# Optimization experiments

Hardware: AMD Instinct MI355X
Metric: run time of the kernel (lower is better)

The kernel has to match this reference:

```python
import jax, jax.numpy as jnp
import numpy as np

EOS_IDX = 2
B, S, T = 512, 64, 32
V, E, H, DENC, L = 128, 256, 512, 1024, 2


def setup_inputs() -> dict:
    key = jax.random.key(0)
    ks = jax.random.split(key, 24)
    s = 0.02
    inp = {
        "encoder_out": jax.random.normal(ks[0], (B, S, DENC), jnp.float32),
        "h0": jax.random.normal(ks[1], (L, B, H), jnp.float32),
        "c0": jax.random.normal(ks[2], (L, B, H), jnp.float32),
        "targets": jax.random.randint(ks[3], (B, T), 0, V),
        "mask": jax.random.randint(ks[4], (B, S), 0, 2).astype(jnp.int32),
        # parameters
        "emb": jax.random.normal(ks[5], (V, E), jnp.float32) * s,
        "W_enc": jax.random.normal(ks[6], (H, DENC), jnp.float32) * s,
        "W_dec": jax.random.normal(ks[7], (H, H), jnp.float32) * s,
        "v": jax.random.normal(ks[8], (H,), jnp.float32) * s,
        "W_ih0": jax.random.normal(ks[9], (4 * H, E + DENC), jnp.float32) * s,
        "W_hh0": jax.random.normal(ks[10], (4 * H, H), jnp.float32) * s,
        "b_ih0": jax.random.normal(ks[11], (4 * H,), jnp.float32) * s,
        "b_hh0": jax.random.normal(ks[12], (4 * H,), jnp.float32) * s,
        "W_ih1": jax.random.normal(ks[13], (4 * H, H), jnp.float32) * s,
        "W_hh1": jax.random.normal(ks[14], (4 * H, H), jnp.float32) * s,
        "b_ih1": jax.random.normal(ks[15], (4 * H,), jnp.float32) * s,
        "b_hh1": jax.random.normal(ks[16], (4 * H,), jnp.float32) * s,
        "W_out": jax.random.normal(ks[17], (V, H + DENC + E), jnp.float32) * s,
        "b_out": jax.random.normal(ks[18], (V,), jnp.float32) * s,
    }
    # guarantee at least one valid source position per row
    inp["mask"] = inp["mask"].at[:, 0].set(1)
    return inp


def _lstm_cell(x, h, c, W_ih, W_hh, b_ih, b_hh):
    gates = x @ W_ih.T + b_ih + h @ W_hh.T + b_hh  # (B, 4H)
    i, f, g, o = jnp.split(gates, 4, axis=-1)      # torch gate order i,f,g,o
    c_new = jax.nn.sigmoid(f) * c + jax.nn.sigmoid(i) * jnp.tanh(g)
    h_new = jax.nn.sigmoid(o) * jnp.tanh(c_new)
    return h_new, c_new


def reference(encoder_out, h0, c0, targets, mask,
              emb, W_enc, W_dec, v,
              W_ih0, W_hh0, b_ih0, b_hh0,
              W_ih1, W_hh1, b_ih1, b_hh1,
              W_out, b_out):
    # teacher_forcing_ratio = 1.0: input tokens are [EOS, targets[:, :-1]]
    tokens = jnp.concatenate(
        [jnp.full((targets.shape[0], 1), EOS_IDX, dtype=targets.dtype),
         targets[:, :-1]], axis=1)                       # (B, T)
    embedded = emb[tokens]                               # (B, T, E)
    enc_proj = jnp.einsum('bsd,hd->bsh', encoder_out, W_enc)  # precompute W_enc(encoder_out)
    mask_b = mask > 0                                    # (B, S)

    def step(carry, x_emb):                              # x_emb: (B, E)
        h, c = carry                                     # each (L, B, H)
        h_top = h[-1]                                    # (B, H)
        dec_proj = h_top @ W_dec.T                       # (B, H)
        energy = jnp.tanh(dec_proj[:, None, :] + enc_proj)   # (B, S, H)
        score = jnp.einsum('bsh,h->bs', energy, v)       # (B, S)
        score = jnp.where(mask_b, score, -jnp.inf)
        weights = jax.nn.softmax(score, axis=-1)         # (B, S)
        context = jnp.einsum('bs,bsd->bd', weights, encoder_out)  # (B, DENC)
        x = jnp.concatenate([x_emb, context], axis=-1)   # (B, E+DENC)
        h0n, c0n = _lstm_cell(x, h[0], c[0], W_ih0, W_hh0, b_ih0, b_hh0)
        h1n, c1n = _lstm_cell(h0n, h[1], c[1], W_ih1, W_hh1, b_ih1, b_hh1)
        pred = jnp.concatenate([h1n, context, x_emb], axis=-1) @ W_out.T + b_out  # (B, V)
        return (jnp.stack([h0n, h1n]), jnp.stack([c0n, c1n])), pred

    (_, _), preds = jax.lax.scan(step, (h0, c0), jnp.swapaxes(embedded, 0, 1))
    return jnp.swapaxes(preds, 0, 1)                     # (B, T, V)
```

## Files before the change

### kernel.cpp

```cpp
#include <hip/hip_runtime.h>
#include <math.h>

#define BB 512
#define SS 64
#define TT 32
#define VV 128
#define EE 256
#define HH 512
#define DENC 1024
#define BH (BB*HH)
#define XW0 1792
#define XW1 1024
#define PW  1792
#define G4H 2048

typedef __attribute__((ext_vector_type(8))) short bf16x8;
typedef __attribute__((ext_vector_type(4))) short bf16x4;
typedef __attribute__((ext_vector_type(4))) float f32x4;

__device__ __forceinline__ float sigf(float x){ return 1.f/(1.f+expf(-x)); }
__device__ __forceinline__ float bf2f(short s){
  return __uint_as_float(((unsigned)(unsigned short)s) << 16);
}
__device__ __forceinline__ short f2bf(float f){
  unsigned u = __float_as_uint(f);
  return (short)((u + 0x7FFF + ((u>>16)&1)) >> 16);
}
__device__ __forceinline__ float tanh_fast(float x){
  x = fminf(fmaxf(x, -15.f), 15.f);
  float e = __expf(2.f*x);
  return (e - 1.f) / (e + 1.f);
}

template<int BM, int BN>
struct GemmPipe {
  static constexpr int LA = 72;
  static __device__ __forceinline__ void run(short* Asb, short* Bsb,
      const short* __restrict__ A, const short* __restrict__ Bt, int K,
      int rowBase, int colBase, int tid, f32x4 acc[BM/32][BN/32])
  {
    constexpr int FI = BM/32, FJ = BN/32, ACH = BM/32, BCH = BN/32;
    const int lane = tid & 63, wave = tid >> 6;
    const int ml = lane & 15, kq = lane >> 4;
    const int wm = (wave >> 1)*(BM/2), wn = (wave & 1)*(BN/2);
    const int arow = (tid*ACH) >> 3, acol = ((tid*ACH) & 7)*8;
    const int brow = (tid*BCH) >> 3, bcol = ((tid*BCH) & 7)*8;
    const short* Ap = A + (size_t)(rowBase+arow)*K + acol;
    const short* Bp = Bt + (size_t)(colBase+brow)*K + bcol;
    bf16x8 ar[ACH], br[BCH];
    #pragma unroll
    for (int c = 0; c < ACH; ++c) ar[c] = *(const bf16x8*)(Ap + c*8);
    #pragma unroll
    for (int c = 0; c < BCH; ++c) br[c] = *(const bf16x8*)(Bp + c*8);
    const int nIter = K >> 6;
    for (int i = 0; i < nIter; ++i) {
      short* Ab = Asb + (i&1)*(BM*LA);
      short* Bb = Bsb + (i&1)*(BN*LA);
      #pragma unroll
      for (int c = 0; c < ACH; ++c) *(bf16x8*)&Ab[arow*LA + acol + c*8] = ar[c];
      #pragma unroll
      for (int c = 0; c < BCH; ++c) *(bf16x8*)&Bb[brow*LA + bcol + c*8] = br[c];
      __syncthreads();
      if (i+1 < nIter) {
        const short* An = Ap + (size_t)(i+1)*64;
        const short* Bn = Bp + (size_t)(i+1)*64;
        #pragma unroll
        for (int c = 0; c < ACH; ++c) ar[c] = *(const bf16x8*)(An + c*8);
        #pragma unroll
        for (int c = 0; c < BCH; ++c) br[c] = *(const bf16x8*)(Bn + c*8);
      }
      #pragma unroll
      for (int kh = 0; kh < 2; ++kh) {
        bf16x8 af[FI], bfv[FJ];
        #pragma unroll
        for (int ii = 0; ii < FI; ++ii)
          af[ii] = *(const bf16x8*)&Ab[(wm + ii*16 + ml)*LA + kh*32 + kq*8];
        #pragma unroll
        for (int jj = 0; jj < FJ; ++jj)
          bfv[jj] = *(const bf16x8*)&Bb[(wn + jj*16 + ml)*LA + kh*32 + kq*8];
        #pragma unroll
        for (int ii = 0; ii < FI; ++ii)
          #pragma unroll
          for (int jj = 0; jj < FJ; ++jj)
            acc[ii][jj] = __builtin_amdgcn_mfma_f32_16x16x32_bf16(af[ii], bfv[jj], acc[ii][jj], 0,0,0);
      }
    }
    __syncthreads();
  }
};

__global__ __launch_bounds__(256)
void gates_fused(const short* __restrict__ A, const short* __restrict__ W,
                 const float* __restrict__ bias, float* __restrict__ cb,
                 short* __restrict__ d1, short* __restrict__ d2, short* __restrict__ d3,
                 int K, int layer)
{
  __shared__ __align__(16) char smem[36864];
  short* As = (short*)smem;
  short* Bs = (short*)(smem + 18432);
  const int tid = threadIdx.x;
  const int rowBase = blockIdx.y*64, colBase = blockIdx.x*64;
  f32x4 acc[2][2];
  #pragma unroll
  for (int i = 0; i < 2; ++i)
    #pragma unroll
    for (int j = 0; j < 2; ++j) acc[i][j] = {0.f,0.f,0.f,0.f};
  GemmPipe<64,64>::run(As, Bs, A, W, K, rowBase, colBase, tid, acc);
  const int lane = tid & 63, wave = tid >> 6, ml = lane & 15, kq = lane >> 4;
  const int wm = (wave >> 1)*32, wn = (wave & 1)*32;
  float* Ct = (float*)smem;
  float bj0 = bias[colBase + wn + ml];
  float bj1 = bias[colBase + wn + 16 + ml];
  #pragma unroll
  for (int ii = 0; ii < 2; ++ii)
    #pragma unroll
    for (int jj = 0; jj < 2; ++jj)
      #pragma unroll
      for (int r2 = 0; r2 < 4; ++r2)
        Ct[(wm + ii*16 + kq*4 + r2)*68 + wn + jj*16 + ml] = acc[ii][jj][r2] + (jj ? bj1 : bj0);
  __syncthreads();
  #pragma unroll
  for (int kk = 0; kk < 4; ++kk) {
    int cidx = tid + kk*256;
    int m = cidx >> 4, hl = cidx & 15;
    float4 gv = *(float4*)&Ct[m*68 + hl*4];
    int b_ = rowBase + m, h_ = (colBase >> 2) + hl;
    float cp = cb[b_*HH + h_];
    float cn = sigf(gv.y)*cp + sigf(gv.x)*tanhf(gv.z);
    float hn = sigf(gv.w)*tanhf(cn);
    cb[b_*HH + h_] = cn;
    short hb16 = f2bf(hn);
    if (layer == 0) {
      d1[(size_t)b_*XW1 + h_] = hb16;
      d2[(size_t)b_*XW0 + h_] = hb16;
    } else {
      d1[(size_t)b_*XW1 + h_] = hb16;
      d2[(size_t)b_*PW  + h_] = hb16;
      d3[(size_t)b_*HH  + h_] = hb16;
    }
  }
}

__global__ __launch_bounds__(256)
void attn_out(const short* __restrict__ enc_proj, const short* __restrict__ enc_out,
              const float* __restrict__ vvec, const int* __restrict__ mask,
              const int* __restrict__ targets, const short* __restrict__ embb,
              const short* __restrict__ hb, const short* __restrict__ wdecT,
              short* __restrict__ xcat0, short* __restrict__ predcat,
              const short* __restrict__ predprev, const short* __restrict__ wout,
              const float* __restrict__ b_out, float* __restrict__ out, int t)
{
  __shared__ __align__(16) char smem[36864];
  const int tid = threadIdx.x;
  if (blockIdx.x >= 256) {
    if (t == 0) return;
    short* As = (short*)smem;
    short* Bs = (short*)(smem + 18432);
    int idx = blockIdx.x - 256;
    int rowBase = (idx >> 1)*64, colBase = (idx & 1)*64;
    f32x4 acc[2][2];
    #pragma unroll
    for (int i = 0; i < 2; ++i)
      #pragma unroll
      for (int j = 0; j < 2; ++j) acc[i][j] = {0.f,0.f,0.f,0.f};
    GemmPipe<64,64>::run(As, Bs, predprev, wout, PW, rowBase, colBase, tid, acc);
    const int lane = tid & 63, wave = tid >> 6, ml = lane & 15, kq = lane >> 4;
    const int wm = (wave >> 1)*32, wn = (wave & 1)*32;
    #pragma unroll
    for (int ii = 0; ii < 2; ++ii)
      #pragma unroll
      for (int jj = 0; jj < 2; ++jj) {
        int n = colBase + wn + jj*16 + ml;
        float bv = b_out[n];
        #pragma unroll
        for (int r2 = 0; r2 < 4; ++r2) {
          int m = rowBase + wm + ii*16 + kq*4 + r2;
          out[(size_t)m*(TT*VV) + (size_t)(t-1)*VV + n] = acc[ii][jj][r2] + bv;
        }
      }
    return;
  }
  if (t >= TT) return;
  const int b0 = blockIdx.x*2;
  float* hbf = (float*)smem;
  float* dps = (float*)(smem + 4096);
  float* vvf = (float*)(smem + 12288);
  float* sc  = (float*)(smem + 14336);
  float* wt  = (float*)(smem + 14848);
  {
    bf16x4 h4 = *(const bf16x4*)&hb[(size_t)b0*HH + tid*4];
    #pragma unroll
    for (int j = 0; j < 4; ++j) hbf[tid*4 + j] = bf2f(h4[j]);
    vvf[tid] = vvec[tid];
    vvf[256 + tid] = vvec[256 + tid];
  }
  __syncthreads();
  {
    int unit = tid & 127, ksel = tid >> 7;
    int bb = unit >> 6, h8 = unit & 63;
    const short* wp = wdecT + (size_t)(ksel*256)*HH + h8*8;
    const float* hrow = hbf + bb*HH + ksel*256;
    float a[8] = {0.f,0.f,0.f,0.f,0.f,0.f,0.f,0.f};
    for (int k = 0; k < 256; ++k) {
      bf16x8 w8 = *(const bf16x8*)(wp + (size_t)k*HH);
      float x = hrow[k];
      #pragma unroll
      for (int j = 0; j < 8; ++j) a[j] += x * bf2f(w8[j]);
    }
    float* d = dps + (ksel*2 + bb)*HH + h8*8;
    #pragma unroll
    for (int j = 0; j < 8; ++j) d[j] = a[j];
  }
  __syncthreads();
  {
    int bb = tid >> 7, h0 = (tid & 127)*4;
    f32x4 s0 = *(f32x4*)&dps[bb*HH + h0];
    f32x4 s1 = *(f32x4*)&dps[(2 + bb)*HH + h0];
    *(f32x4*)&dps[bb*HH + h0] = s0 + s1;
  }
  __syncthreads();
  {
    int u = tid >> 1, khalf = tid & 1;
    int bb = u >> 6, s = u & 63;
    const short* ep = enc_proj + ((size_t)(b0+bb)*SS + s)*HH + khalf*256;
    const float* dpp = dps + bb*HH + khalf*256;
    const float* vp  = vvf + khalf*256;
    float accv = 0.f;
    for (int hc = 0; hc < 32; ++hc) {
      bf16x8 e8 = *(const bf16x8*)(ep + hc*8);
      f32x4 d0 = *(const f32x4*)(dpp + hc*8);
      f32x4 d1 = *(const f32x4*)(dpp + hc*8 + 4);
      f32x4 v0 = *(const f32x4*)(vp + hc*8);
      f32x4 v1 = *(const f32x4*)(vp + hc*8 + 4);
      #pragma unroll
      for (int j = 0; j < 4; ++j) accv += v0[j]*tanh_fast(d0[j] + bf2f(e8[j]));
      #pragma unroll
      for (int j = 0; j < 4; ++j) accv += v1[j]*tanh_fast(d1[j] + bf2f(e8[4+j]));
    }
    accv += __shfl_xor(accv, 1, 64);
    if (khalf == 0) sc[bb*64 + s] = accv;
  }
  __syncthreads();
  if (tid < 128) {
    int bb = tid >> 6, s = tid & 63;
    int valid = mask[(b0+bb)*SS + s];
    float x = valid ? sc[bb*64 + s] : -INFINITY;
    float mx = x;
    #pragma unroll
    for (int off = 32; off; off >>= 1) mx = fmaxf(mx, __shfl_xor(mx, off, 64));
    float e = valid ? __expf(x - mx) : 0.f;
    float sum = e;
    #pragma unroll
    for (int off = 32; off; off >>= 1) sum += __shfl_xor(sum, off, 64);
    wt[bb*64 + s] = e / sum;
  }
  __syncthreads();
  {
    int bb = tid >> 7, d0 = (tid & 127)*8;
    const short* eob = enc_out + (size_t)(b0+bb)*SS*DENC + d0;
    float ca[8] = {0.f,0.f,0.f,0.f,0.f,0.f,0.f,0.f};
    for (int s = 0; s < SS; ++s) {
      float w = wt[bb*64 + s];
      bf16x8 e8 = *(const bf16x8*)(eob + (size_t)s*DENC);
      #pragma unroll
      for (int j = 0; j < 8; ++j) ca[j] += w * bf2f(e8[j]);
    }
    bf16x8 cb8;
    #pragma unroll
    for (int j = 0; j < 8; ++j) cb8[j] = f2bf(ca[j]);
    int b_ = b0 + bb;
    *(bf16x8*)&xcat0[(size_t)b_*XW0 + EE + d0] = cb8;
    *(bf16x8*)&predcat[(size_t)b_*PW + HH + d0] = cb8;
  }
  #pragma unroll
  for (int bb = 0; bb < 2; ++bb) {
    int b_ = b0 + bb;
    int tok = (t == 0) ? 2 : targets[b_*TT + t - 1];
    short ev = embb[tok*EE + tid];
    xcat0[(size_t)b_*XW0 + tid] = ev;
    predcat[(size_t)b_*PW + HH + DENC + tid] = ev;
  }
}

__global__ __launch_bounds__(256)
void enc_gemm(short* __restrict__ C, const short* __restrict__ A, const short* __restrict__ Bt,
              int K, int ldc)
{
  __shared__ __align__(16) char smem[55296];
  short* As = (short*)smem;
  short* Bs = (short*)(smem + 18432);
  const int tid = threadIdx.x;
  const int rowBase = blockIdx.y*64, colBase = blockIdx.x*128;
  f32x4 acc[2][4];
  #pragma unroll
  for (int i = 0; i < 2; ++i)
    #pragma unroll
    for (int j = 0; j < 4; ++j) acc[i][j] = {0.f,0.f,0.f,0.f};
  GemmPipe<64,128>::run(As, Bs, A, Bt, K, rowBase, colBase, tid, acc);
  const int lane = tid & 63, wave = tid >> 6, ml = lane & 15, kq = lane >> 4;
  const int wm = (wave >> 1)*32, wn = (wave & 1)*64;
  #pragma unroll
  for (int ii = 0; ii < 2; ++ii)
    #pragma unroll
    for (int jj = 0; jj < 4; ++jj) {
      int n = colBase + wn + jj*16 + ml;
      #pragma unroll
      for (int r2 = 0; r2 < 4; ++r2) {
        int m = rowBase + wm + ii*16 + kq*4 + r2;
        C[(size_t)m*ldc + n] = f2bf(acc[ii][jj][r2]);
      }
    }
}

__global__ __launch_bounds__(256)
void build_wcat_bf(short* __restrict__ wcat0, short* __restrict__ wcat1,
                   const float* __restrict__ wih0, const float* __restrict__ whh0,
                   const float* __restrict__ wih1, const float* __restrict__ whh1)
{
  int idx = blockIdx.x*256 + threadIdx.x;
  const int N0 = G4H*XW0;
  if (idx < N0) {
    int n = idx / XW0, k = idx % XW0;
    int row = (n & 3)*HH + (n >> 2);
    float v = (k < EE+DENC) ? wih0[(size_t)row*(EE+DENC) + k] : whh0[(size_t)row*HH + (k - (EE+DENC))];
    wcat0[idx] = f2bf(v);
  } else {
    int j = idx - N0;
    int n = j / XW1, k = j % XW1;
    int row = (n & 3)*HH + (n >> 2);
    float v = (k < HH) ? wih1[(size_t)row*HH + k] : whh1[(size_t)row*HH + (k - HH)];
    wcat1[j] = f2bf(v);
  }
}

__global__ __launch_bounds__(256)
void cvt_encout(short* __restrict__ dst, const float* __restrict__ src)
{
  size_t i8 = ((size_t)blockIdx.x*256 + threadIdx.x)*8;
  float4 a = *(const float4*)&src[i8];
  float4 b = *(const float4*)&src[i8+4];
  bf16x8 o;
  o[0]=f2bf(a.x); o[1]=f2bf(a.y); o[2]=f2bf(a.z); o[3]=f2bf(a.w);
  o[4]=f2bf(b.x); o[5]=f2bf(b.y); o[6]=f2bf(b.z); o[7]=f2bf(b.w);
  *(bf16x8*)&dst[i8] = o;
}

__global__ __launch_bounds__(256)
void prep_misc(float* __restrict__ cbuf, short* __restrict__ xcat0a, short* __restrict__ xcat1a,
               short* __restrict__ hb, short* __restrict__ wdecT, short* __restrict__ wenc,
               short* __restrict__ wout, short* __restrict__ embb,
               float* __restrict__ bias0i, float* __restrict__ bias1i,
               const float* __restrict__ c0, const float* __restrict__ h0,
               const float* __restrict__ W_dec, const float* __restrict__ W_enc,
               const float* __restrict__ W_out, const float* __restrict__ emb,
               const float* __restrict__ b_ih0, const float* __restrict__ b_hh0,
               const float* __restrict__ b_ih1, const float* __restrict__ b_hh1)
{
  int idx = blockIdx.x*256 + threadIdx.x;
  if (idx < 524288) { cbuf[idx] = c0[idx]; return; }
  idx -= 524288;
  if (idx < 262144) {
    int b = idx >> 9, h = idx & 511;
    xcat0a[(size_t)b*XW0 + EE + DENC + h] = f2bf(h0[idx]);
    return;
  }
  idx -= 262144;
  if (idx < 262144) {
    int b = idx >> 9, h = idx & 511;
    short v = f2bf(h0[BH + idx]);
    xcat1a[(size_t)b*XW1 + HH + h] = v;
    hb[idx] = v;
    return;
  }
  idx -= 262144;
  if (idx < 262144) {
    int k = idx >> 9, n = idx & 511;
    wdecT[idx] = f2bf(W_dec[(size_t)n*HH + k]);
    return;
  }
  idx -= 262144;
  if (idx < 524288) { wenc[idx] = f2bf(W_enc[idx]); return; }
  idx -= 524288;
  if (idx < 229376) { wout[idx] = f2bf(W_out[idx]); return; }
  idx -= 229376;
  if (idx < 32768)  { embb[idx] = f2bf(emb[idx]); return; }
  idx -= 32768;
  if (idx < 2048) {
    int row = (idx & 3)*HH + (idx >> 2);
    bias0i[idx] = b_ih0[row] + b_hh0[row];
    return;
  }
  idx -= 2048;
  {
    int row = (idx & 3)*HH + (idx >> 2);
    bias1i[idx] = b_ih1[row] + b_hh1[row];
  }
}

extern "C" void kernel_launch(void* const* d_in, const int* in_sizes, int n_in,
                              void* d_out, int out_size, void* d_ws, size_t ws_size,
                              hipStream_t stream) {
  const float* enc_out = (const float*)d_in[0];
  const float* h0      = (const float*)d_in[1];
  const float* c0      = (const float*)d_in[2];
  const int*   targets = (const int*)d_in[3];
  const int*   mask    = (const int*)d_in[4];
  const float* emb     = (const float*)d_in[5];
  const float* W_enc   = (const float*)d_in[6];
  const float* W_dec   = (const float*)d_in[7];
  const float* v       = (const float*)d_in[8];
  const float* b_ih0   = (const float*)d_in[11];
  const float* b_hh0   = (const float*)d_in[12];
  const float* b_ih1   = (const float*)d_in[15];
  const float* b_hh1   = (const float*)d_in[16];
  const float* b_out   = (const float*)d_in[18];
  float* out = (float*)d_out;

  char* ws = (char*)d_ws;
  size_t o = 0;
  short* enc_out_bf = (short*)(ws + o); o += (size_t)BB*SS*DENC*2;
  short* enc_proj_bf= (short*)(ws + o); o += (size_t)BB*SS*HH*2;
  short* wcat0i     = (short*)(ws + o); o += (size_t)G4H*XW0*2;
  short* wcat1i     = (short*)(ws + o); o += (size_t)G4H*XW1*2;
  short* wdecT      = (short*)(ws + o); o += (size_t)HH*HH*2;
  short* wenc_bf    = (short*)(ws + o); o += (size_t)HH*DENC*2;
  short* wout_bf    = (short*)(ws + o); o += (size_t)VV*PW*2;
  short* emb_bf     = (short*)(ws + o); o += (size_t)VV*EE*2;
  short* xcat0a     = (short*)(ws + o); o += (size_t)BB*XW0*2;
  short* xcat0b     = (short*)(ws + o); o += (size_t)BB*XW0*2;
  short* xcat1a     = (short*)(ws + o); o += (size_t)BB*XW1*2;
  short* xcat1b     = (short*)(ws + o); o += (size_t)BB*XW1*2;
  short* predcata   = (short*)(ws + o); o += (size_t)BB*PW*2;
  short* predcatb   = (short*)(ws + o); o += (size_t)BB*PW*2;
  short* hb         = (short*)(ws + o); o += (size_t)BH*2;
  float* cbuf       = (float*)(ws + o); o += (size_t)2*BH*4;
  float* bias0i     = (float*)(ws + o); o += (size_t)G4H*4;
  float* bias1i     = (float*)(ws + o); o += (size_t)G4H*4;
  (void)ws_size; (void)in_sizes; (void)n_in; (void)out_size;

  cvt_encout<<<16384, 256, 0, stream>>>(enc_out_bf, enc_out);
  build_wcat_bf<<<22528, 256, 0, stream>>>(wcat0i, wcat1i,
      (const float*)d_in[9], (const float*)d_in[10], (const float*)d_in[13], (const float*)d_in[14]);
  prep_misc<<<8208, 256, 0, stream>>>(cbuf, xcat0a, xcat1a, hb, wdecT, wenc_bf, wout_bf, emb_bf,
      bias0i, bias1i, c0, h0, W_dec, W_enc, (const float*)d_in[17], emb,
      b_ih0, b_hh0, b_ih1, b_hh1);
  enc_gemm<<<dim3(HH/128, (BB*SS)/64), 256, 0, stream>>>(
      enc_proj_bf, enc_out_bf, wenc_bf, DENC, HH);

  short* xc0[2] = {xcat0a, xcat0b};
  short* xc1[2] = {xcat1a, xcat1b};
  short* pc[2]  = {predcata, predcatb};
  for (int t = 0; t < TT; ++t) {
    attn_out<<<272, 256, 0, stream>>>(enc_proj_bf, enc_out_bf, v, mask, targets, emb_bf,
        hb, wdecT, xc0[t&1], pc[t&1], pc[(t+1)&1], wout_bf, b_out, out, t);
    gates_fused<<<dim3(G4H/64, BB/64), 256, 0, stream>>>(
        xc0[t&1], wcat0i, bias0i, cbuf, xc1[t&1], xc0[(t+1)&1] + EE + DENC, (short*)nullptr, XW0, 0);
    gates_fused<<<dim3(G4H/64, BB/64), 256, 0, stream>>>(
        xc1[t&1], wcat1i, bias1i, cbuf + BH, xc1[(t+1)&1] + HH, pc[t&1], hb, XW1, 1);
  }
  attn_out<<<272, 256, 0, stream>>>(enc_proj_bf, enc_out_bf, v, mask, targets, emb_bf,
      hb, wdecT, xc0[0], pc[0], pc[1], wout_bf, b_out, out, TT);
}
```

Baseline: 2.868 ms.

## Fuse decoder time loop into one persistent kernel with grid barriers

Replaces the 97 per-step kernel launches with a single persistent kernel of 256 blocks that runs all 32 timesteps. Phases are separated by an atomic-counter grid barrier. The output projection is reworked into a split-K MFMA over 16x16 tiles so it maps onto the same 256 blocks. The aim is to remove launch overhead and inter-kernel gaps on this latency-bound recurrence. In exchange it relies on all 256 blocks being co-resident and adds barrier spin cost at each phase.

```diff
diff --git a/kernel.cpp b/kernel.cpp
--- a/kernel.cpp
+++ b/kernel.cpp
@@ -30,6 +30,23 @@
   x = fminf(fmaxf(x, -15.f), 15.f);
   float e = __expf(2.f*x);
   return (e - 1.f) / (e + 1.f);
+}
+
+__device__ __forceinline__ void gridbar(unsigned* cnt, unsigned* gen)
+{
+  __syncthreads();
+  if (threadIdx.x == 0) {
+    unsigned g = __hip_atomic_load(gen, __ATOMIC_RELAXED, __HIP_MEMORY_SCOPE_AGENT);
+    unsigned old = __hip_atomic_fetch_add(cnt, 1u, __ATOMIC_ACQ_REL, __HIP_MEMORY_SCOPE_AGENT);
+    if (old == 255u) {
+      __hip_atomic_store(cnt, 0u, __ATOMIC_RELAXED, __HIP_MEMORY_SCOPE_AGENT);
+      __hip_atomic_store(gen, g + 1u, __ATOMIC_RELEASE, __HIP_MEMORY_SCOPE_AGENT);
+    } else {
+      while (__hip_atomic_load(gen, __ATOMIC_ACQUIRE, __HIP_MEMORY_SCOPE_AGENT) == g)
+        __builtin_amdgcn_s_sleep(1);
+    }
+  }
+  __syncthreads();
 }
 
 template<int BM, int BN>
@@ -89,17 +106,15 @@
   }
 };
 
-__global__ __launch_bounds__(256)
-void gates_fused(const short* __restrict__ A, const short* __restrict__ W,
-                 const float* __restrict__ bias, float* __restrict__ cb,
-                 short* __restrict__ d1, short* __restrict__ d2, short* __restrict__ d3,
-                 int K, int layer)
-{
-  __shared__ __align__(16) char smem[36864];
+__device__ __forceinline__ void gates_phase(char* smem, int tid, int blk,
+    const short* __restrict__ A, const short* __restrict__ W,
+    const float* __restrict__ bias, float* __restrict__ cb,
+    short* __restrict__ d1, short* __restrict__ d2, short* __restrict__ d3,
+    int K, int layer)
+{
   short* As = (short*)smem;
   short* Bs = (short*)(smem + 18432);
-  const int tid = threadIdx.x;
-  const int rowBase = blockIdx.y*64, colBase = blockIdx.x*64;
+  const int rowBase = (blk >> 5)*64, colBase = (blk & 31)*64;
   f32x4 acc[2][2];
   #pragma unroll
   for (int i = 0; i < 2; ++i)
@@ -141,47 +156,14 @@
   }
 }
 
-__global__ __launch_bounds__(256)
-void attn_out(const short* __restrict__ enc_proj, const short* __restrict__ enc_out,
-              const float* __restrict__ vvec, const int* __restrict__ mask,
-              const int* __restrict__ targets, const short* __restrict__ embb,
-              const short* __restrict__ hb, const short* __restrict__ wdecT,
-              short* __restrict__ xcat0, short* __restrict__ predcat,
-              const short* __restrict__ predprev, const short* __restrict__ wout,
-              const float* __restrict__ b_out, float* __restrict__ out, int t)
-{
-  __shared__ __align__(16) char smem[36864];
-  const int tid = threadIdx.x;
-  if (blockIdx.x >= 256) {
-    if (t == 0) return;
-    short* As = (short*)smem;
-    short* Bs = (short*)(smem + 18432);
-    int idx = blockIdx.x - 256;
-    int rowBase = (idx >> 1)*64, colBase = (idx & 1)*64;
-    f32x4 acc[2][2];
-    #pragma unroll
-    for (int i = 0; i < 2; ++i)
-      #pragma unroll
-      for (int j = 0; j < 2; ++j) acc[i][j] = {0.f,0.f,0.f,0.f};
-    GemmPipe<64,64>::run(As, Bs, predprev, wout, PW, rowBase, colBase, tid, acc);
-    const int lane = tid & 63, wave = tid >> 6, ml = lane & 15, kq = lane >> 4;
-    const int wm = (wave >> 1)*32, wn = (wave & 1)*32;
-    #pragma unroll
-    for (int ii = 0; ii < 2; ++ii)
-      #pragma unroll
-      for (int jj = 0; jj < 2; ++jj) {
-        int n = colBase + wn + jj*16 + ml;
-        float bv = b_out[n];
-        #pragma unroll
-        for (int r2 = 0; r2 < 4; ++r2) {
-          int m = rowBase + wm + ii*16 + kq*4 + r2;
-          out[(size_t)m*(TT*VV) + (size_t)(t-1)*VV + n] = acc[ii][jj][r2] + bv;
-        }
-      }
-    return;
-  }
-  if (t >= TT) return;
-  const int b0 = blockIdx.x*2;
+__device__ __forceinline__ void attn_phase(char* smem, int tid, int blk,
+    const short* __restrict__ enc_proj, const short* __restrict__ enc_out,
+    const float* __restrict__ vvec, const int* __restrict__ mask,
+    const int* __restrict__ targets, const short* __restrict__ embb,
+    const short* __restrict__ hb, const short* __restrict__ wdecT,
+    short* __restrict__ xcat0, short* __restrict__ predcat, int t)
+{
+  const int b0 = blk*2;
   float* hbf = (float*)smem;
   float* dps = (float*)(smem + 4096);
   float* vvf = (float*)(smem + 12288);
@@ -282,13 +264,79 @@
   }
 }
 
+__device__ __forceinline__ void out_phase(char* smem, int tid, int blk,
+    const short* __restrict__ pred, const short* __restrict__ wout,
+    const float* __restrict__ b_out, float* __restrict__ out, int tprev)
+{
+  __syncthreads();
+  const int lane = tid & 63, wave = tid >> 6;
+  const int m0 = (blk >> 3)*16, n0 = (blk & 7)*16;
+  const int ml = lane & 15, kq = lane >> 4;
+  f32x4 acc = {0.f,0.f,0.f,0.f};
+  const short* Ap = pred + (size_t)(m0 + ml)*PW + wave*448 + kq*8;
+  const short* Bp = wout + (size_t)(n0 + ml)*PW + wave*448 + kq*8;
+  #pragma unroll 4
+  for (int kk = 0; kk < 14; ++kk) {
+    bf16x8 a8 = *(const bf16x8*)(Ap + kk*32);
+    bf16x8 b8 = *(const bf16x8*)(Bp + kk*32);
+    acc = __builtin_amdgcn_mfma_f32_16x16x32_bf16(a8, b8, acc, 0,0,0);
+  }
+  float* red = (float*)smem;
+  *(f32x4*)&red[wave*256 + lane*4] = acc;
+  __syncthreads();
+  if (wave == 0) {
+    f32x4 s = *(f32x4*)&red[lane*4];
+    #pragma unroll
+    for (int w = 1; w < 4; ++w) s += *(f32x4*)&red[w*256 + lane*4];
+    float bv = b_out[n0 + ml];
+    #pragma unroll
+    for (int r = 0; r < 4; ++r)
+      out[(size_t)(m0 + kq*4 + r)*(TT*VV) + (size_t)tprev*VV + n0 + ml] = s[r] + bv;
+  }
+  __syncthreads();
+}
+
+__global__ __launch_bounds__(256)
+void persist(const short* __restrict__ enc_proj, const short* __restrict__ enc_out,
+             const float* __restrict__ vvec, const int* __restrict__ mask,
+             const int* __restrict__ targets, const short* __restrict__ embb,
+             short* __restrict__ hb, const short* __restrict__ wdecT,
+             short* xc0a, short* xc0b, short* xc1a, short* xc1b,
+             short* pca, short* pcb,
+             const short* __restrict__ wcat0, const short* __restrict__ wcat1,
+             const float* __restrict__ bias0, const float* __restrict__ bias1,
+             float* __restrict__ cbuf,
+             const short* __restrict__ wout, const float* __restrict__ b_out,
+             float* __restrict__ out, unsigned* __restrict__ bar)
+{
+  __shared__ __align__(16) char smem[36864];
+  const int tid = threadIdx.x, blk = blockIdx.x;
+  unsigned* cnt = bar; unsigned* gen = bar + 1;
+  short* xc0[2] = {xc0a, xc0b};
+  short* xc1[2] = {xc1a, xc1b};
+  short* pc2[2] = {pca, pcb};
+  for (int t = 0; t < TT; ++t) {
+    attn_phase(smem, tid, blk, enc_proj, enc_out, vvec, mask, targets, embb,
+               hb, wdecT, xc0[t&1], pc2[t&1], t);
+    if (t > 0) out_phase(smem, tid, blk, pc2[(t+1)&1], wout, b_out, out, t-1);
+    gridbar(cnt, gen);
+    gates_phase(smem, tid, blk, xc0[t&1], wcat0, bias0, cbuf, xc1[t&1],
+                xc0[(t+1)&1] + EE + DENC, (short*)nullptr, XW0, 0);
+    gridbar(cnt, gen);
+    gates_phase(smem, tid, blk, xc1[t&1], wcat1, bias1, cbuf + BH, xc1[(t+1)&1] + HH,
+                pc2[t&1], hb, XW1, 1);
+    gridbar(cnt, gen);
+  }
+  out_phase(smem, tid, blk, pc2[1], wout, b_out, out, TT-1);
+}
+
 __global__ __launch_bounds__(256)
 void enc_gemm(short* __restrict__ C, const short* __restrict__ A, const short* __restrict__ Bt,
               int K, int ldc)
 {
-  __shared__ __align__(16) char smem[55296];
-  short* As = (short*)smem;
-  short* Bs = (short*)(smem + 18432);
+  __shared__ __align__(16) char smem2[55296];
+  short* As = (short*)smem2;
+  short* Bs = (short*)(smem2 + 18432);
   const int tid = threadIdx.x;
   const int rowBase = blockIdx.y*64, colBase = blockIdx.x*128;
   f32x4 acc[2][4];
@@ -350,6 +398,7 @@
                short* __restrict__ hb, short* __restrict__ wdecT, short* __restrict__ wenc,
                short* __restrict__ wout, short* __restrict__ embb,
                float* __restrict__ bias0i, float* __restrict__ bias1i,
+               unsigned* __restrict__ bar,
                const float* __restrict__ c0, const float* __restrict__ h0,
                const float* __restrict__ W_dec, const float* __restrict__ W_enc,
                const float* __restrict__ W_out, const float* __restrict__ emb,
@@ -391,10 +440,13 @@
     return;
   }
   idx -= 2048;
-  {
+  if (idx < 2048) {
     int row = (idx & 3)*HH + (idx >> 2);
     bias1i[idx] = b_ih1[row] + b_hh1[row];
-  }
+    return;
+  }
+  idx -= 2048;
+  if (idx < 2) bar[idx] = 0u;
 }
 
 extern "C" void kernel_launch(void* const* d_in, const int* in_sizes, int n_in,
@@ -436,28 +488,19 @@
   float* cbuf       = (float*)(ws + o); o += (size_t)2*BH*4;
   float* bias0i     = (float*)(ws + o); o += (size_t)G4H*4;
   float* bias1i     = (float*)(ws + o); o += (size_t)G4H*4;
+  unsigned* bar     = (unsigned*)(ws + o); o += 256;
   (void)ws_size; (void)in_sizes; (void)n_in; (void)out_size;
 
   cvt_encout<<<16384, 256, 0, stream>>>(enc_out_bf, enc_out);
   build_wcat_bf<<<22528, 256, 0, stream>>>(wcat0i, wcat1i,
       (const float*)d_in[9], (const float*)d_in[10], (const float*)d_in[13], (const float*)d_in[14]);
-  prep_misc<<<8208, 256, 0, stream>>>(cbuf, xcat0a, xcat1a, hb, wdecT, wenc_bf, wout_bf, emb_bf,
-      bias0i, bias1i, c0, h0, W_dec, W_enc, (const float*)d_in[17], emb,
+  prep_misc<<<8209, 256, 0, stream>>>(cbuf, xcat0a, xcat1a, hb, wdecT, wenc_bf, wout_bf, emb_bf,
+      bias0i, bias1i, bar, c0, h0, W_dec, W_enc, (const float*)d_in[17], emb,
       b_ih0, b_hh0, b_ih1, b_hh1);
   enc_gemm<<<dim3(HH/128, (BB*SS)/64), 256, 0, stream>>>(
       enc_proj_bf, enc_out_bf, wenc_bf, DENC, HH);
 
-  short* xc0[2] = {xcat0a, xcat0b};
-  short* xc1[2] = {xcat1a, xcat1b};
-  short* pc[2]  = {predcata, predcatb};
-  for (int t = 0; t < TT; ++t) {
-    attn_out<<<272, 256, 0, stream>>>(enc_proj_bf, enc_out_bf, v, mask, targets, emb_bf,
-        hb, wdecT, xc0[t&1], pc[t&1], pc[(t+1)&1], wout_bf, b_out, out, t);
-    gates_fused<<<dim3(G4H/64, BB/64), 256, 0, stream>>>(
-        xc0[t&1], wcat0i, bias0i, cbuf, xc1[t&1], xc0[(t+1)&1] + EE + DENC, (short*)nullptr, XW0, 0);
-    gates_fused<<<dim3(G4H/64, BB/64), 256, 0, stream>>>(
-        xc1[t&1], wcat1i, bias1i, cbuf + BH, xc1[(t+1)&1] + HH, pc[t&1], hb, XW1, 1);
-  }
-  attn_out<<<272, 256, 0, stream>>>(enc_proj_bf, enc_out_bf, v, mask, targets, emb_bf,
-      hb, wdecT, xc0[0], pc[0], pc[1], wout_bf, b_out, out, TT);
-}
+  persist<<<256, 256, 0, stream>>>(enc_proj_bf, enc_out_bf, v, mask, targets, emb_bf,
+      hb, wdecT, xcat0a, xcat0b, xcat1a, xcat1b, predcata, predcatb,
+      wcat0i, wcat1i, bias0i, bias1i, cbuf, wout_bf, b_out, out, bar);
+}
```

New measurement: 7.081 ms. +146.9%, slower.
